# Performance work log

Measured on AMD Instinct MI355X. Metric: run time of the kernel, lower is better.

The kernel has to match this reference:

```python
import jax, jax.numpy as jnp
import numpy as np

B, T, D = 8, 2048, 512
DK = 128
FENETRES = (24, 168, 720)
EPS = 1e-5


def setup_inputs() -> dict:
    key = jax.random.key(0)
    ks = jax.random.split(key, 8)
    s = 0.02
    return {
        "x": jax.random.normal(ks[0], (B, T, D), dtype=jnp.float32),
        "Wq": jax.random.normal(ks[1], (D, DK), dtype=jnp.float32) * s,
        "bq": jnp.zeros((DK,), dtype=jnp.float32),
        "Wk": jax.random.normal(ks[2], (D, DK), dtype=jnp.float32) * s,
        "bk": jnp.zeros((DK,), dtype=jnp.float32),
        "Wo": jax.random.normal(ks[3], (D, D), dtype=jnp.float32) * s,
        "bo": jnp.zeros((D,), dtype=jnp.float32),
        "gamma": jnp.ones((D,), dtype=jnp.float32),
        "beta": jnp.zeros((D,), dtype=jnp.float32),
    }


def reference(x, Wq, bq, Wk, bk, Wo, bo, gamma, beta):
    # projections (dropout is identity in eval mode)
    q = x @ Wq + bq                      # [B,T,DK]
    k = x @ Wk + bk                      # [B,T,DK]
    dk = q.shape[-1]
    # scores are identical across window scales; compute once
    scores = jnp.einsum('btd,bsd->bts', q, k) / jnp.sqrt(jnp.float32(dk))
    t = jnp.arange(x.shape[1])
    dist = jnp.abs(t[:, None] - t[None, :])  # [T,T]
    acc = jnp.zeros_like(x)
    for w in FENETRES:
        band = dist <= (w // 2)              # row i attends to [i-w//2, i+w//2]
        s = jnp.where(band[None, :, :], scores, jnp.float32(-1e9))
        attn = jax.nn.softmax(s, axis=-1)    # [B,T,T]
        acc = acc + jnp.einsum('bts,bsd->btd', attn, x)
    acc = acc / jnp.float32(len(FENETRES))
    out = acc @ Wo + bo
    res = x + out
    # LayerNorm over last dim, eps=1e-5
    mu = jnp.mean(res, axis=-1, keepdims=True)
    var = jnp.mean(jnp.square(res - mu), axis=-1, keepdims=True)
    return (res - mu) * jax.lax.rsqrt(var + EPS) * gamma + beta
```

## Files before the change

### kernel.cpp

```cpp
#include <hip/hip_runtime.h>

typedef unsigned short u16;
typedef __attribute__((ext_vector_type(4))) unsigned short u16x4;
typedef __attribute__((ext_vector_type(8))) unsigned short u16x8;
typedef __attribute__((ext_vector_type(8))) short bf16x8;
typedef __attribute__((ext_vector_type(4))) float f32x4;

constexpr int Bn = 8, Tn = 2048, Dn = 512, DKn = 128;
constexpr int QB = 64;
constexpr int WJ = 832;
constexpr int NCH = 13;
constexpr int WQB = 16;
constexpr int WST = 776;

__device__ inline u16 f2bf(float f) {
  unsigned u = __float_as_uint(f);
  return (u16)((u + 0x7FFFu + ((u >> 16) & 1u)) >> 16);
}
__device__ inline float bf2f(u16 h) {
  return __uint_as_float(((unsigned)h) << 16);
}
__device__ inline void gload16(const void* g, void* l) {
  __builtin_amdgcn_global_load_lds(
      (const __attribute__((address_space(1))) unsigned int*)g,
      (__attribute__((address_space(3))) unsigned int*)l, 16, 0, 0);
}
__device__ inline f32x4 mfma16(bf16x8 a, bf16x8 b, f32x4 c) {
  return __builtin_amdgcn_mfma_f32_16x16x32_bf16(a, b, c, 0, 0, 0);
}

__global__ __launch_bounds__(256) void xpose_kernel(
    const float* __restrict__ x, u16* __restrict__ xT, u16* __restrict__ xbf) {
  __shared__ u16 tile[64][72];
  const int blk = blockIdx.x;
  const int b = blk >> 8;
  const int rem = blk & 255;
  const int t0 = (rem >> 3) * 64, d0 = (rem & 7) * 64;
  const int tid = threadIdx.x;

#pragma unroll
  for (int it = 0; it < 4; ++it) {
    int r = (tid >> 4) + it * 16;
    int c = (tid & 15) * 4;
    float4 v = *(const float4*)&x[(size_t)(b * Tn + t0 + r) * Dn + d0 + c];
    u16 b0 = f2bf(v.x), b1 = f2bf(v.y), b2 = f2bf(v.z), b3 = f2bf(v.w);
    tile[c + 0][r] = b0;
    tile[c + 1][r] = b1;
    tile[c + 2][r] = b2;
    tile[c + 3][r] = b3;
    u16x4 pv; pv[0] = b0; pv[1] = b1; pv[2] = b2; pv[3] = b3;
    *(u16x4*)&xbf[(size_t)(b * Tn + t0 + r) * Dn + d0 + c] = pv;
  }
  __syncthreads();
  const int dr = tid >> 2, ts = (tid & 3) * 16;
  u16x8 v0 = *(const u16x8*)&tile[dr][ts];
  u16x8 v1 = *(const u16x8*)&tile[dr][ts + 8];
  u16* dst = xT + (size_t)(b * Dn + d0 + dr) * Tn + t0 + ts;
  *(u16x8*)dst = v0;
  *(u16x8*)(dst + 8) = v1;
}

__global__ __launch_bounds__(256) void wprep_kernel(
    const float* __restrict__ Wq, const float* __restrict__ Wk,
    const float* __restrict__ Wo,
    u16* __restrict__ WqkT, u16* __restrict__ WoT) {
  __shared__ u16 tile[64][72];
  const int tid = threadIdx.x;
  const int blk = blockIdx.x;
  const float* src; u16* dst;
  int srcC, r0, c0, rowOff;
  if (blk < 32) {
    src = (blk < 16) ? Wq : Wk;
    rowOff = (blk < 16) ? 0 : 128;
    int t = blk & 15;
    r0 = (t >> 1) * 64; c0 = (t & 1) * 64;
    srcC = 128; dst = WqkT;
  } else {
    int t = blk - 32;
    src = Wo; rowOff = 0;
    r0 = (t >> 3) * 64; c0 = (t & 7) * 64;
    srcC = 512; dst = WoT;
  }
#pragma unroll
  for (int it = 0; it < 4; ++it) {
    int r = (tid >> 4) + it * 16;
    int c = (tid & 15) * 4;
    float4 v = *(const float4*)&src[(size_t)(r0 + r) * srcC + c0 + c];
    tile[c + 0][r] = f2bf(v.x);
    tile[c + 1][r] = f2bf(v.y);
    tile[c + 2][r] = f2bf(v.z);
    tile[c + 3][r] = f2bf(v.w);
  }
  __syncthreads();
  const int dr = tid >> 2, ts = (tid & 3) * 16;
  u16x8 v0 = *(const u16x8*)&tile[dr][ts];
  u16x8 v1 = *(const u16x8*)&tile[dr][ts + 8];
  u16* dp = dst + (size_t)(rowOff + c0 + dr) * 512 + r0 + ts;
  *(u16x8*)dp = v0;
  *(u16x8*)(dp + 8) = v1;
}

__global__ __launch_bounds__(512) void qk_mfma_kernel(
    const u16* __restrict__ xbf, const u16* __restrict__ WqkT,
    const float* __restrict__ bq, const float* __restrict__ bk,
    u16* __restrict__ qbf, u16* __restrict__ kbf) {
  __shared__ u16 as_[2][64 * 64];
  __shared__ u16 bs_[2][256 * 64];
  const int tid = threadIdx.x, w = tid >> 6, l = tid & 63;
  const int r0 = blockIdx.x * 64;
  const int wr = w >> 2, wc = w & 3;

  f32x4 acc[2][4];
#pragma unroll
  for (int mm = 0; mm < 2; ++mm)
#pragma unroll
    for (int n = 0; n < 4; ++n) acc[mm][n] = (f32x4){0.f, 0.f, 0.f, 0.f};

  auto stageA = [&](int c, int buf) {
    int row = 8 * w + (l >> 3);
    int ss = (l & 7) ^ (row & 7);
    gload16(xbf + ((size_t)(r0 + row) * Dn + c * 64 + ss * 8),
            (char*)&as_[buf][0] + w * 1024);
  };
  auto stageB = [&](int c, int buf) {
#pragma unroll
    for (int ii = 0; ii < 4; ++ii) {
      int i = 4 * w + ii;
      int n = i * 8 + (l >> 3);
      int ss = (l & 7) ^ (n & 7);
      gload16(WqkT + ((size_t)n * Dn + c * 64 + ss * 8),
              (char*)&bs_[buf][0] + i * 1024);
    }
  };
  stageA(0, 0); stageB(0, 0);
  __syncthreads();
  for (int c = 0; c < 8; ++c) {
    if (c + 1 < 8) { stageA(c + 1, (c + 1) & 1); stageB(c + 1, (c + 1) & 1); }
    const u16* ab = &as_[c & 1][0];
    const u16* bb = &bs_[c & 1][0];
#pragma unroll
    for (int kk = 0; kk < 2; ++kk) {
      int rA0 = wr * 32 + (l & 15);
      int sA = ((l >> 4) + 4 * kk) ^ (rA0 & 7);
      bf16x8 a0 = *(const bf16x8*)(ab + rA0 * 64 + sA * 8);
      bf16x8 a1 = *(const bf16x8*)(ab + (rA0 + 16) * 64 + sA * 8);
#pragma unroll
      for (int n = 0; n < 4; ++n) {
        int rB = wc * 64 + n * 16 + (l & 15);
        int sB = ((l >> 4) + 4 * kk) ^ (rB & 7);
        bf16x8 bv = *(const bf16x8*)(bb + rB * 64 + sB * 8);
        acc[0][n] = mfma16(a0, bv, acc[0][n]);
        acc[1][n] = mfma16(a1, bv, acc[1][n]);
      }
    }
    __syncthreads();
  }
#pragma unroll
  for (int n = 0; n < 4; ++n) {
    int col = wc * 64 + n * 16 + (l & 15);
    float bias = (col < 128) ? bq[col] : bk[col - 128];
    u16* outp = (col < 128) ? (qbf + col) : (kbf + col - 128);
#pragma unroll
    for (int mm = 0; mm < 2; ++mm)
#pragma unroll
      for (int i = 0; i < 4; ++i) {
        int row = r0 + wr * 32 + mm * 16 + 4 * (l >> 4) + i;
        outp[(size_t)row * DKn] = f2bf(acc[mm][n][i] + bias);
      }
  }
}

__global__ __launch_bounds__(256) void weights_kernel(
    const u16* __restrict__ qbf, const u16* __restrict__ kbf,
    u16* __restrict__ Wg) {
  __shared__ u16 S[WQB * WST];
  __shared__ float spart[4][WQB][3];
  const int tid = threadIdx.x, w = tid >> 6, l = tid & 63;
  const int blk = (blockIdx.x & 7) * 128 + (blockIdx.x >> 3);
  const int b = blk >> 7;
  const int tt = blk & 127;
  const int t0 = tt * WQB;
  const int jbase = t0 - 360;
  const float scale = 0.08838834764831845f;

  bf16x8 a[4];
  {
    int row = t0 + (l & 15);
    const u16* qp = qbf + (size_t)(b * Tn + row) * DKn + (l >> 4) * 8;
#pragma unroll
    for (int kk = 0; kk < 4; ++kk) a[kk] = *(const bf16x8*)(qp + kk * 32);
  }

  float s0[4], s1[4], s2[4];
#pragma unroll
  for (int i = 0; i < 4; ++i) { s0[i] = 0.f; s1[i] = 0.f; s2[i] = 0.f; }
  const int rbase = 4 * (l >> 4);

  for (int c = 0; c < 12; ++c) {
    int jj = c * 64 + w * 16 + (l & 15);
    int j = jbase + jj;
    int jc = j < 0 ? 0 : (j > Tn - 1 ? Tn - 1 : j);
    const u16* kp = kbf + (size_t)(b * Tn + jc) * DKn + (l >> 4) * 8;
    f32x4 acc = {0.f, 0.f, 0.f, 0.f};
#pragma unroll
    for (int kk = 0; kk < 4; ++kk)
      acc = mfma16(a[kk], *(const bf16x8*)(kp + kk * 32), acc);
    bool valid = (j >= 0) && (j < Tn);
#pragma unroll
    for (int i = 0; i < 4; ++i) {
      int r = rbase + i;
      int dist = jj - r - 360; dist = dist < 0 ? -dist : dist;
      float e = __expf(acc[i] * scale);
      e = (valid && dist <= 360) ? e : 0.f;
      S[r * WST + jj] = f2bf(e);
      bool in0 = dist <= 12, in1 = dist <= 84;
      s0[i] += in0 ? e : 0.f;
      s1[i] += (in1 && !in0) ? e : 0.f;
      s2[i] += in1 ? 0.f : e;
    }
  }

#pragma unroll
  for (int o = 1; o < 16; o <<= 1)
#pragma unroll
    for (int i = 0; i < 4; ++i) {
      s0[i] += __shfl_xor(s0[i], o);
      s1[i] += __shfl_xor(s1[i], o);
      s2[i] += __shfl_xor(s2[i], o);
    }
  if ((l & 15) == 0) {
#pragma unroll
    for (int i = 0; i < 4; ++i) {
      spart[w][rbase + i][0] = s0[i];
      spart[w][rbase + i][1] = s1[i];
      spart[w][rbase + i][2] = s2[i];
    }
  }
  __syncthreads();

  const int off = (tt & 3) * 16;
  const int pvblk = b * 32 + (tt >> 2);
#pragma unroll
  for (int rr = 0; rr < 4; ++rr) {
    int r = 4 * w + rr;
    float L0 = spart[0][r][0] + spart[1][r][0] + spart[2][r][0] + spart[3][r][0];
    float L1 = L0 + spart[0][r][1] + spart[1][r][1] + spart[2][r][1] + spart[3][r][1];
    float L2 = L1 + spart[0][r][2] + spart[1][r][2] + spart[2][r][2] + spart[3][r][2];
    float F2 = (1.f / 3.f) / L2;
    float F1 = (1.f / 3.f) / L1 + F2;
    float F0 = (1.f / 3.f) / L0 + F1;
    const int center = r + 360;
    u16* wrow = Wg + ((size_t)pvblk * QB + off + r) * WJ;
#pragma unroll
    for (int t = 0; t < 6; ++t) {
      int jjw = 2 * l + 128 * t;
      if (jjw < 736) {
        unsigned pv2 = *(const unsigned*)&S[r * WST + jjw];
        float e0 = bf2f((u16)(pv2 & 0xffff));
        float e1 = bf2f((u16)(pv2 >> 16));
        int d0 = jjw - center; d0 = d0 < 0 ? -d0 : d0;
        int d1 = jjw + 1 - center; d1 = d1 < 0 ? -d1 : d1;
        float c0 = e0 * (d0 <= 12 ? F0 : (d0 <= 84 ? F1 : F2));
        float c1 = e1 * (d1 <= 12 ? F0 : (d1 <= 84 ? F1 : F2));
        unsigned o2 = (unsigned)f2bf(c0) | ((unsigned)f2bf(c1) << 16);
        *(unsigned*)&wrow[off + jjw] = o2;
      }
    }
    if (l < 48) {
      int jjp = (l < (off >> 1)) ? 2 * l : 736 + 2 * l;
      *(unsigned*)&wrow[jjp] = 0u;
    }
  }
}

__global__ __launch_bounds__(512) void pv_kernel(
    const u16* __restrict__ Wg, const u16* __restrict__ xT,
    u16* __restrict__ accbf) {
  __shared__ u16 xs[2][256 * 64];
  __shared__ u16 ws[2][QB * 64];
  const int tid = threadIdx.x;
  const int w = tid >> 6, l = tid & 63;
  const int work = (blockIdx.x & 7) * 64 + (blockIdx.x >> 3);
  const int b = work >> 6;
  const int rem = work & 63;
  const int tt = rem >> 1;
  const int dh = rem & 1;
  const int t064 = tt * QB;
  const int jbase = t064 - 360;
  const int pvblk = b * 32 + tt;
  const int wr = w >> 2, wc = w & 3;

  f32x4 acc[2][4];
#pragma unroll
  for (int mm = 0; mm < 2; ++mm)
#pragma unroll
    for (int n = 0; n < 4; ++n) acc[mm][n] = (f32x4){0.f,0.f,0.f,0.f};

  auto stage = [&](int c, int buf) {
#pragma unroll
    for (int ii = 0; ii < 4; ++ii) {
      int i = 4 * w + ii;
      int d = i * 8 + (l >> 3);
      int ss = (l & 7) ^ (d & 7);
      int g = jbase + c * 64 + ss * 8;
      g = g < 0 ? 0 : (g > Tn - 8 ? Tn - 8 : g);
      gload16(xT + ((size_t)(b * Dn + dh * 256 + d) * Tn + g),
              (char*)&xs[buf][0] + i * 1024);
    }
    int row = 8 * w + (l >> 3);
    int ss = (l & 7) ^ (row & 7);
    gload16(Wg + ((size_t)(pvblk * QB + row)) * WJ + c * 64 + ss * 8,
            (char*)&ws[buf][0] + w * 1024);
  };

  stage(0, 0);
  __syncthreads();
  for (int c = 0; c < NCH; ++c) {
    if (c + 1 < NCH) stage(c + 1, (c + 1) & 1);
    const u16* xb = &xs[c & 1][0];
    const u16* wb = &ws[c & 1][0];
#pragma unroll
    for (int kk = 0; kk < 2; ++kk) {
      int rA0 = wr * 32 + (l & 15);
      int sA = ((l >> 4) + 4 * kk) ^ (rA0 & 7);
      bf16x8 a0 = *(const bf16x8*)(wb + rA0 * 64 + sA * 8);
      bf16x8 a1 = *(const bf16x8*)(wb + (rA0 + 16) * 64 + sA * 8);
#pragma unroll
      for (int n = 0; n < 4; ++n) {
        int rB = wc * 64 + n * 16 + (l & 15);
        int sB = ((l >> 4) + 4 * kk) ^ (rB & 7);
        bf16x8 bv = *(const bf16x8*)(xb + rB * 64 + sB * 8);
        acc[0][n] = mfma16(a0, bv, acc[0][n]);
        acc[1][n] = mfma16(a1, bv, acc[1][n]);
      }
    }
    __syncthreads();
  }
#pragma unroll
  for (int mm = 0; mm < 2; ++mm)
#pragma unroll
    for (int n = 0; n < 4; ++n)
#pragma unroll
      for (int i = 0; i < 4; ++i) {
        int row = wr * 32 + mm * 16 + 4 * (l >> 4) + i;
        int col = dh * 256 + wc * 64 + n * 16 + (l & 15);
        accbf[(size_t)(b * Tn + t064 + row) * Dn + col] = f2bf(acc[mm][n][i]);
      }
}

__global__ __launch_bounds__(512, 4) void out_ln_mfma_kernel(
    const u16* __restrict__ accbf, const float* __restrict__ x,
    const u16* __restrict__ WoT, const float* __restrict__ bo,
    const float* __restrict__ gamma, const float* __restrict__ beta,
    float* __restrict__ out) {
  __shared__ u16 as_[2][32 * 32];
  __shared__ u16 bs_[2][512 * 32];
  __shared__ float red[32][8][2];
  const int tid = threadIdx.x, w = tid >> 6, l = tid & 63;
  const int r0 = blockIdx.x * 32;

  f32x4 acc[4][2];
#pragma unroll
  for (int m = 0; m < 4; ++m)
#pragma unroll
    for (int nh = 0; nh < 2; ++nh) acc[m][nh] = (f32x4){0.f,0.f,0.f,0.f};

  auto stageA = [&](int c, int buf) {
    if (w < 2) {
      int i = w * 64 + l;
      int row = i >> 2;
      int ss = (i & 3) ^ ((row >> 1) & 3);
      gload16(accbf + ((size_t)(r0 + row) * Dn + c * 32 + ss * 8),
              (char*)&as_[buf][0] + w * 1024);
    }
  };
  auto stageB = [&](int c, int buf) {
#pragma unroll
    for (int ii = 0; ii < 4; ++ii) {
      int i = ii * 8 + w;
      int n = i * 16 + (l >> 2);
      int ss = (l & 3) ^ ((n >> 1) & 3);
      gload16(WoT + ((size_t)n * Dn + c * 32 + ss * 8),
              (char*)&bs_[buf][0] + i * 1024);
    }
  };

  stageA(0, 0); stageB(0, 0);
  __syncthreads();
  for (int c = 0; c < 16; ++c) {
    if (c + 1 < 16) { stageA(c + 1, (c + 1) & 1); stageB(c + 1, (c + 1) & 1); }
    const u16* ab = &as_[c & 1][0];
    const u16* bb = &bs_[c & 1][0];
    bf16x8 bfr[2];
#pragma unroll
    for (int nh = 0; nh < 2; ++nh) {
      int rB = nh * 16 + (l & 15);
      int sB = (l >> 4) ^ ((rB >> 1) & 3);
      bfr[nh] = *(const bf16x8*)(ab + rB * 32 + sB * 8);
    }
#pragma unroll
    for (int m = 0; m < 4; ++m) {
      int rA = w * 64 + m * 16 + (l & 15);
      int sA = (l >> 4) ^ ((rA >> 1) & 3);
      bf16x8 afr = *(const bf16x8*)(bb + rA * 32 + sA * 8);
      acc[m][0] = mfma16(afr, bfr[0], acc[m][0]);
      acc[m][1] = mfma16(afr, bfr[1], acc[m][1]);
    }
    __syncthreads();
  }

  float s[2] = {0.f, 0.f}, s2[2] = {0.f, 0.f};
#pragma unroll
  for (int nh = 0; nh < 2; ++nh) {
    int trow_g = r0 + nh * 16 + (l & 15);
#pragma unroll
    for (int m = 0; m < 4; ++m) {
      int outc = w * 64 + m * 16 + (l >> 4) * 4;
      float4 xq  = *(const float4*)&x[(size_t)trow_g * Dn + outc];
      float4 bo4 = *(const float4*)&bo[outc];
      acc[m][nh][0] += bo4.x + xq.x;
      acc[m][nh][1] += bo4.y + xq.y;
      acc[m][nh][2] += bo4.z + xq.z;
      acc[m][nh][3] += bo4.w + xq.w;
#pragma unroll
      for (int i = 0; i < 4; ++i) {
        float v = acc[m][nh][i];
        s[nh] += v; s2[nh] += v * v;
      }
    }
  }
#pragma unroll
  for (int nh = 0; nh < 2; ++nh) {
    s[nh]  += __shfl_xor(s[nh], 16);  s[nh]  += __shfl_xor(s[nh], 32);
    s2[nh] += __shfl_xor(s2[nh], 16); s2[nh] += __shfl_xor(s2[nh], 32);
  }
  if (l < 16) {
#pragma unroll
    for (int nh = 0; nh < 2; ++nh) {
      red[nh * 16 + l][w][0] = s[nh];
      red[nh * 16 + l][w][1] = s2[nh];
    }
  }
  __syncthreads();
#pragma unroll
  for (int nh = 0; nh < 2; ++nh) {
    int trow = nh * 16 + (l & 15);
    float ts = 0.f, ts2 = 0.f;
#pragma unroll
    for (int ww = 0; ww < 8; ++ww) {
      ts  += red[trow][ww][0];
      ts2 += red[trow][ww][1];
    }
    float mean = ts * (1.f / 512.f);
    float var  = ts2 * (1.f / 512.f) - mean * mean;
    float inv  = rsqrtf(var + 1e-5f);
    size_t grow = (size_t)(r0 + trow) * Dn;
#pragma unroll
    for (int m = 0; m < 4; ++m) {
      int outc = w * 64 + m * 16 + (l >> 4) * 4;
      float4 g4  = *(const float4*)&gamma[outc];
      float4 be4 = *(const float4*)&beta[outc];
      float4 o4;
      o4.x = (acc[m][nh][0] - mean) * inv * g4.x + be4.x;
      o4.y = (acc[m][nh][1] - mean) * inv * g4.y + be4.y;
      o4.z = (acc[m][nh][2] - mean) * inv * g4.z + be4.z;
      o4.w = (acc[m][nh][3] - mean) * inv * g4.w + be4.w;
      *(float4*)&out[grow + outc] = o4;
    }
  }
}

extern "C" void kernel_launch(void* const* d_in, const int* in_sizes, int n_in,
                              void* d_out, int out_size, void* d_ws, size_t ws_size,
                              hipStream_t stream) {
  const float* x     = (const float*)d_in[0];
  const float* Wq    = (const float*)d_in[1];
  const float* bq    = (const float*)d_in[2];
  const float* Wk    = (const float*)d_in[3];
  const float* bk    = (const float*)d_in[4];
  const float* Wo    = (const float*)d_in[5];
  const float* bo    = (const float*)d_in[6];
  const float* gamma = (const float*)d_in[7];
  const float* beta  = (const float*)d_in[8];
  float* out = (float*)d_out;

  u16* qbf   = (u16*)d_ws;
  u16* kbf   = qbf   + (size_t)Bn * Tn * DKn;
  u16* xT    = kbf   + (size_t)Bn * Tn * DKn;
  u16* xbf   = xT    + (size_t)Bn * Dn * Tn;
  u16* Wg    = xbf   + (size_t)Bn * Tn * Dn;
  u16* accbf = Wg    + (size_t)Bn * 32 * QB * WJ;
  u16* WqkT  = accbf + (size_t)Bn * Tn * Dn;
  u16* WoT   = WqkT  + (size_t)256 * 512;

  xpose_kernel<<<Bn * 256, 256, 0, stream>>>(x, xT, xbf);
  wprep_kernel<<<96, 256, 0, stream>>>(Wq, Wk, Wo, WqkT, WoT);
  qk_mfma_kernel<<<Bn * Tn / 64, 512, 0, stream>>>(xbf, WqkT, bq, bk, qbf, kbf);
  weights_kernel<<<Bn * 128, 256, 0, stream>>>(qbf, kbf, Wg);
  pv_kernel<<<Bn * 64, 512, 0, stream>>>(Wg, xT, accbf);
  out_ln_mfma_kernel<<<Bn * Tn / 32, 512, 0, stream>>>(accbf, x, WoT, bo, gamma, beta, out);
}
```

Measured before the change: 116.8 us.

## Pre-swizzle Wo into MFMA fragment layout and load operands directly from global

wprep now writes Wo in a fragment-ordered layout so each lane's bf16x8 MFMA operand is one contiguous 16-byte load. The output/LayerNorm GEMM drops its LDS double-buffered staging and per-iteration barriers, and reads both Wo and the attention accumulator straight from global memory (relying on cache). This removes LDS traffic and synchronisation. In exchange, loads are repeated across blocks through cache, and global latency is exposed without explicit prefetch.

```diff
diff --git a/kernel.cpp b/kernel.cpp
--- a/kernel.cpp
+++ b/kernel.cpp
@@ -63,23 +63,23 @@
 __global__ __launch_bounds__(256) void wprep_kernel(
     const float* __restrict__ Wq, const float* __restrict__ Wk,
     const float* __restrict__ Wo,
-    u16* __restrict__ WqkT, u16* __restrict__ WoT) {
+    u16* __restrict__ WqkT, u16* __restrict__ WoTf) {
   __shared__ u16 tile[64][72];
   const int tid = threadIdx.x;
   const int blk = blockIdx.x;
-  const float* src; u16* dst;
+  const float* src;
   int srcC, r0, c0, rowOff;
   if (blk < 32) {
     src = (blk < 16) ? Wq : Wk;
     rowOff = (blk < 16) ? 0 : 128;
     int t = blk & 15;
     r0 = (t >> 1) * 64; c0 = (t & 1) * 64;
-    srcC = 128; dst = WqkT;
+    srcC = 128;
   } else {
     int t = blk - 32;
     src = Wo; rowOff = 0;
     r0 = (t >> 3) * 64; c0 = (t & 7) * 64;
-    srcC = 512; dst = WoT;
+    srcC = 512;
   }
 #pragma unroll
   for (int it = 0; it < 4; ++it) {
@@ -95,9 +95,20 @@
   const int dr = tid >> 2, ts = (tid & 3) * 16;
   u16x8 v0 = *(const u16x8*)&tile[dr][ts];
   u16x8 v1 = *(const u16x8*)&tile[dr][ts + 8];
-  u16* dp = dst + (size_t)(rowOff + c0 + dr) * 512 + r0 + ts;
-  *(u16x8*)dp = v0;
-  *(u16x8*)(dp + 8) = v1;
+  if (blk < 32) {
+    u16* dp = WqkT + (size_t)(rowOff + c0 + dr) * 512 + r0 + ts;
+    *(u16x8*)dp = v0;
+    *(u16x8*)(dp + 8) = v1;
+  } else {
+    int n = c0 + dr;
+    int d0 = r0 + ts, d1 = d0 + 8;
+    size_t a0 = (size_t)(((n >> 4) * 16 + (d0 >> 5)) * 64 +
+                         ((((d0 >> 3) & 3) << 4) | (n & 15))) * 8;
+    size_t a1 = (size_t)(((n >> 4) * 16 + (d1 >> 5)) * 64 +
+                         ((((d1 >> 3) & 3) << 4) | (n & 15))) * 8;
+    *(u16x8*)&WoTf[a0] = v0;
+    *(u16x8*)&WoTf[a1] = v1;
+  }
 }
 
 __global__ __launch_bounds__(512) void qk_mfma_kernel(
@@ -350,11 +361,9 @@
 
 __global__ __launch_bounds__(512, 4) void out_ln_mfma_kernel(
     const u16* __restrict__ accbf, const float* __restrict__ x,
-    const u16* __restrict__ WoT, const float* __restrict__ bo,
+    const u16* __restrict__ WoTf, const float* __restrict__ bo,
     const float* __restrict__ gamma, const float* __restrict__ beta,
     float* __restrict__ out) {
-  __shared__ u16 as_[2][32 * 32];
-  __shared__ u16 bs_[2][512 * 32];
   __shared__ float red[32][8][2];
   const int tid = threadIdx.x, w = tid >> 6, l = tid & 63;
   const int r0 = blockIdx.x * 32;
@@ -365,48 +374,21 @@
 #pragma unroll
     for (int nh = 0; nh < 2; ++nh) acc[m][nh] = (f32x4){0.f,0.f,0.f,0.f};
 
-  auto stageA = [&](int c, int buf) {
-    if (w < 2) {
-      int i = w * 64 + l;
-      int row = i >> 2;
-      int ss = (i & 3) ^ ((row >> 1) & 3);
-      gload16(accbf + ((size_t)(r0 + row) * Dn + c * 32 + ss * 8),
-              (char*)&as_[buf][0] + w * 1024);
-    }
-  };
-  auto stageB = [&](int c, int buf) {
-#pragma unroll
-    for (int ii = 0; ii < 4; ++ii) {
-      int i = ii * 8 + w;
-      int n = i * 16 + (l >> 2);
-      int ss = (l & 3) ^ ((n >> 1) & 3);
-      gload16(WoT + ((size_t)n * Dn + c * 32 + ss * 8),
-              (char*)&bs_[buf][0] + i * 1024);
-    }
-  };
-
-  stageA(0, 0); stageB(0, 0);
-  __syncthreads();
+  const u16* aptr = WoTf + (size_t)(w * 4) * 16 * 512 + l * 8;
+  const u16* bptr = accbf + (size_t)(r0 + (l & 15)) * Dn + (l >> 4) * 8;
+
+#pragma unroll 4
   for (int c = 0; c < 16; ++c) {
-    if (c + 1 < 16) { stageA(c + 1, (c + 1) & 1); stageB(c + 1, (c + 1) & 1); }
-    const u16* ab = &as_[c & 1][0];
-    const u16* bb = &bs_[c & 1][0];
     bf16x8 bfr[2];
 #pragma unroll
-    for (int nh = 0; nh < 2; ++nh) {
-      int rB = nh * 16 + (l & 15);
-      int sB = (l >> 4) ^ ((rB >> 1) & 3);
-      bfr[nh] = *(const bf16x8*)(ab + rB * 32 + sB * 8);
-    }
+    for (int nh = 0; nh < 2; ++nh)
+      bfr[nh] = *(const bf16x8*)(bptr + (size_t)nh * 16 * Dn + c * 32);
 #pragma unroll
     for (int m = 0; m < 4; ++m) {
-      int rA = w * 64 + m * 16 + (l & 15);
-      int sA = (l >> 4) ^ ((rA >> 1) & 3);
-      bf16x8 afr = *(const bf16x8*)(bb + rA * 32 + sA * 8);
+      bf16x8 afr = *(const bf16x8*)(aptr + (size_t)(m * 16 + c) * 512);
       acc[m][0] = mfma16(afr, bfr[0], acc[m][0]);
       acc[m][1] = mfma16(afr, bfr[1], acc[m][1]);
     }
-    __syncthreads();
   }
 
   float s[2] = {0.f, 0.f}, s2[2] = {0.f, 0.f};
@@ -491,12 +473,12 @@
   u16* Wg    = xbf   + (size_t)Bn * Tn * Dn;
   u16* accbf = Wg    + (size_t)Bn * 32 * QB * WJ;
   u16* WqkT  = accbf + (size_t)Bn * Tn * Dn;
-  u16* WoT   = WqkT  + (size_t)256 * 512;
+  u16* WoTf  = WqkT  + (size_t)256 * 512;
 
   xpose_kernel<<<Bn * 256, 256, 0, stream>>>(x, xT, xbf);
-  wprep_kernel<<<96, 256, 0, stream>>>(Wq, Wk, Wo, WqkT, WoT);
+  wprep_kernel<<<96, 256, 0, stream>>>(Wq, Wk, Wo, WqkT, WoTf);
   qk_mfma_kernel<<<Bn * Tn / 64, 512, 0, stream>>>(xbf, WqkT, bq, bk, qbf, kbf);
   weights_kernel<<<Bn * 128, 256, 0, stream>>>(qbf, kbf, Wg);
   pv_kernel<<<Bn * 64, 512, 0, stream>>>(Wg, xT, accbf);
-  out_ln_mfma_kernel<<<Bn * Tn / 32, 512, 0, stream>>>(accbf, x, WoT, bo, gamma, beta, out);
-}
+  out_ln_mfma_kernel<<<Bn * Tn / 32, 512, 0, stream>>>(accbf, x, WoTf, bo, gamma, beta, out);
+}
```

After: 120.7 us. +3.3%, slower.
